# Kernel optimization log

Hardware: AMD Instinct MI355X
Metric: run time of the kernel (lower is better)

The kernel has to match this reference:

```python
import jax, jax.numpy as jnp
import numpy as np

B, D, H, K = 65536, 256, 256, 11
TEMP = 1.0
EPS = 1e-8  # torch cosine_similarity eps


def _gelu(v):
    return jax.nn.gelu(v, approximate=False)  # torch nn.GELU default is exact


def setup_inputs() -> dict:
    key = jax.random.key(0)
    ks = jax.random.split(key, 9)
    s_d = 1.0 / np.sqrt(D)
    s_h = 1.0 / np.sqrt(H)
    return {
        "x": jax.random.normal(ks[0], (B, D), jnp.float32),
        # K transform MLPs, stacked: D->H (gelu) ->D
        "Tw1": jax.random.normal(ks[1], (K, D, H), jnp.float32) * s_d,
        "Tb1": jax.random.normal(ks[2], (K, H), jnp.float32) * 0.01,
        "Tw2": jax.random.normal(ks[3], (K, H, D), jnp.float32) * s_h,
        "Tb2": jax.random.normal(ks[4], (K, D), jnp.float32) * 0.01,
        # encoder MLP: D->H (gelu) ->H
        "Ew1": jax.random.normal(ks[5], (D, H), jnp.float32) * s_d,
        "Eb1": jax.random.normal(ks[6], (H,), jnp.float32) * 0.01,
        "Ew2": jax.random.normal(ks[7], (H, H), jnp.float32) * s_h,
        "Eb2": jax.random.normal(ks[8], (H,), jnp.float32) * 0.01,
    }


def reference(x, Tw1, Tb1, Tw2, Tb2, Ew1, Eb1, Ew2, Eb2):
    def enc(h):  # [..., D] -> [..., H]; dropout is identity at inference
        return _gelu(h @ Ew1 + Eb1) @ Ew2 + Eb2

    # batched transforms: [K, B, D]
    tx = _gelu(jnp.einsum('bd,kdh->kbh', x, Tw1) + Tb1[:, None, :])
    tx = jnp.einsum('kbh,khd->kbd', tx, Tw2) + Tb2[:, None, :]

    z = enc(x)        # [B, H]
    zt = enc(tx)      # [K, B, H]

    nz = jnp.linalg.norm(z, axis=-1)    # [B]
    nzt = jnp.linalg.norm(zt, axis=-1)  # [K, B]

    # exp(cos(z, z_k) / T)  -> [K, B]
    sim_z = jnp.exp(jnp.einsum('bh,kbh->kb', z, zt)
                    / jnp.maximum(nz[None, :] * nzt, EPS) / TEMP)
    # exp(cos(z_l, z_k) / T) -> [K, K, B]
    S = jnp.exp(jnp.einsum('lbh,kbh->lkb', zt, zt)
                / jnp.maximum(nzt[:, None, :] * nzt[None, :, :], EPS) / TEMP)
    diag = jnp.diagonal(S, axis1=0, axis2=1).T  # [K, B]
    neg = S.sum(axis=0) - diag                  # sum over l != k

    scores = jnp.log(sim_z / (sim_z + neg))     # [K, B]
    return -scores.sum(axis=0)                  # [B]
```

## Files before the change

### kernel.cpp

```cpp
#include <hip/hip_runtime.h>
#include <hip/hip_bf16.h>
#include <stdint.h>

#define BTOT  65536
#define KTR   11
#define NSLOT 12

typedef __attribute__((ext_vector_type(8))) short bf16x8_t;
typedef __attribute__((ext_vector_type(4))) float f32x4_t;

__device__ __forceinline__ int act_addr(int m, int n) {
    return m * 256 + ((((n >> 3) + m) & 31) << 3) + (n & 7);
}

__device__ __forceinline__ float gelu_fast(float x) {
    float x2 = x * x;
    float t2 = 2.3022083f * x * fmaf(0.044715f, x2, 1.0f);
    float e  = exp2f(fminf(t2, 44.f));
    return x * e * __builtin_amdgcn_rcpf(1.0f + e);
}

__global__ void cast_x_kernel(const float* __restrict__ x, __hip_bfloat16* __restrict__ xb) {
    int i = (blockIdx.x * 256 + threadIdx.x) * 4;
    float4 v = *(const float4*)(x + i);
    union { __hip_bfloat16 h[4]; uint64_t u; } o;
    o.h[0] = __float2bfloat16(v.x);
    o.h[1] = __float2bfloat16(v.y);
    o.h[2] = __float2bfloat16(v.z);
    o.h[3] = __float2bfloat16(v.w);
    *(uint64_t*)(xb + i) = o.u;
}

__global__ void transpose_cast_kernel(const float* __restrict__ in,
                                      __hip_bfloat16* __restrict__ out,
                                      int R, int C) {
    __shared__ float tile[32][33];
    int tpc = C >> 5;
    int tr = (blockIdx.x / tpc) << 5;
    int tc = (blockIdx.x % tpc) << 5;
    const float* bi = in + (size_t)blockIdx.y * R * C;
    __hip_bfloat16* bo = out + (size_t)blockIdx.y * R * C;
    int lx = threadIdx.x & 31, ly = threadIdx.x >> 5;
    #pragma unroll
    for (int r = 0; r < 32; r += 8)
        tile[ly + r][lx] = bi[(size_t)(tr + ly + r) * C + tc + lx];
    __syncthreads();
    #pragma unroll
    for (int r = 0; r < 32; r += 8)
        bo[(size_t)(tc + ly + r) * R + tr + lx] = __float2bfloat16(tile[lx][ly + r]);
}

__global__ void fuse_w_kernel(const __hip_bfloat16* __restrict__ Ew1t,
                              const __hip_bfloat16* __restrict__ Tw2b,
                              __hip_bfloat16* __restrict__ Wft)
{
    __shared__ __align__(16) __hip_bfloat16 bt[64 * 256];
    const int tid  = threadIdx.x;
    const int wave = tid >> 6, lane = tid & 63;
    const int lr = lane & 15, q = lane >> 4;
    const int k  = blockIdx.y;
    const int h0 = blockIdx.x << 6;
    const __hip_bfloat16* src = Tw2b + (size_t)k * 65536;

    #pragma unroll
    for (int i = 0; i < 8; ++i) {
        int lin = i * 256 + tid;
        int r = lin >> 5, g = lin & 31;
        bf16x8_t v = *(const bf16x8_t*)(src + (size_t)(h0 + r) * 256 + g * 8);
        *(bf16x8_t*)(bt + act_addr(r, g * 8)) = v;
    }
    __syncthreads();

    const int wc = wave << 6;
    f32x4_t acc[4][4];
    #pragma unroll
    for (int mt = 0; mt < 4; ++mt)
        #pragma unroll
        for (int nt = 0; nt < 4; ++nt)
            acc[mt][nt] = (f32x4_t){0.f, 0.f, 0.f, 0.f};

    #pragma unroll 1
    for (int kc = 0; kc < 8; ++kc) {
        const int kof = (kc << 5) + (q << 3);
        bf16x8_t a[4], b[4];
        #pragma unroll
        for (int mt = 0; mt < 4; ++mt)
            a[mt] = *(const bf16x8_t*)(Ew1t + (size_t)(wc + (mt << 4) + lr) * 256 + kof);
        #pragma unroll
        for (int nt = 0; nt < 4; ++nt)
            b[nt] = *(const bf16x8_t*)(bt + act_addr((nt << 4) + lr, kof));
        #pragma unroll
        for (int mt = 0; mt < 4; ++mt)
            #pragma unroll
            for (int nt = 0; nt < 4; ++nt)
                acc[mt][nt] = __builtin_amdgcn_mfma_f32_16x16x32_bf16(a[mt], b[nt], acc[mt][nt], 0, 0, 0);
    }

    __hip_bfloat16* dst = Wft + (size_t)k * 65536;
    #pragma unroll
    for (int mt = 0; mt < 4; ++mt)
        #pragma unroll
        for (int nt = 0; nt < 4; ++nt) {
            const int h = h0 + (nt << 4) + lr;
            #pragma unroll
            for (int r = 0; r < 4; ++r) {
                const int j = wc + (mt << 4) + (q << 2) + r;
                dst[(size_t)j * 256 + h] = __float2bfloat16(acc[mt][nt][r]);
            }
        }
}

__global__ void fuse_b_kernel(const float* __restrict__ Tb2,
                              const float* __restrict__ Ew1,
                              const float* __restrict__ Eb1,
                              float* __restrict__ bf)
{
    const int k = blockIdx.x, j = threadIdx.x;
    float s = Eb1[j];
    #pragma unroll 4
    for (int d = 0; d < 256; ++d)
        s = fmaf(Tb2[k * 256 + d], Ew1[d * 256 + j], s);
    bf[k * 256 + j] = s;
}

template<bool DO_GELU>
__device__ void run_stage(__hip_bfloat16* act,
                          const __hip_bfloat16* __restrict__ Wt,
                          const float* __restrict__ bias,
                          int wave, int lane)
{
    const int lr = lane & 15;
    const int q  = lane >> 4;
    const int wc = wave << 6;

    f32x4_t acc[4][4];
    #pragma unroll
    for (int mt = 0; mt < 4; ++mt) {
        const float4 bv = *(const float4*)(bias + wc + (mt << 4) + (q << 2));
        #pragma unroll
        for (int nt = 0; nt < 4; ++nt)
            acc[mt][nt] = (f32x4_t){bv.x, bv.y, bv.z, bv.w};
    }

    bf16x8_t a[4];
    #pragma unroll
    for (int mt = 0; mt < 4; ++mt)
        a[mt] = *(const bf16x8_t*)(Wt + (size_t)(wc + (mt << 4) + lr) * 256 + (q << 3));

    #pragma unroll 1
    for (int kc = 0; kc < 8; ++kc) {
        const int kof = (kc << 5) + (q << 3);
        bf16x8_t an[4];
        if (kc < 7) {
            #pragma unroll
            for (int mt = 0; mt < 4; ++mt)
                an[mt] = *(const bf16x8_t*)(Wt + (size_t)(wc + (mt << 4) + lr) * 256 + kof + 32);
        }
        bf16x8_t b[4];
        #pragma unroll
        for (int nt = 0; nt < 4; ++nt)
            b[nt] = *(const bf16x8_t*)(act + act_addr((nt << 4) + lr, kof));
        #pragma unroll
        for (int mt = 0; mt < 4; ++mt)
            #pragma unroll
            for (int nt = 0; nt < 4; ++nt)
                acc[mt][nt] = __builtin_amdgcn_mfma_f32_16x16x32_bf16(a[mt], b[nt], acc[mt][nt], 0, 0, 0);
        if (kc < 7) {
            #pragma unroll
            for (int mt = 0; mt < 4; ++mt) a[mt] = an[mt];
        }
    }

    __syncthreads();
    #pragma unroll
    for (int mt = 0; mt < 4; ++mt) {
        const int nbase = wc + (mt << 4) + (q << 2);
        #pragma unroll
        for (int nt = 0; nt < 4; ++nt) {
            const int row = (nt << 4) + lr;
            union { __hip_bfloat16 h[4]; uint64_t u; } o;
            #pragma unroll
            for (int r = 0; r < 4; ++r) {
                float v = acc[mt][nt][r];
                if (DO_GELU) v = gelu_fast(v);
                o.h[r] = __float2bfloat16(v);
            }
            *(uint64_t*)(act + act_addr(row, nbase)) = o.u;
        }
    }
    __syncthreads();
}

__launch_bounds__(256, 3)
__global__ void chain_kernel(const __hip_bfloat16* __restrict__ xb,
                             const __hip_bfloat16* __restrict__ Tw1t,
                             const float* __restrict__ Tb1,
                             const __hip_bfloat16* __restrict__ Wft,
                             const float* __restrict__ bfb,
                             const __hip_bfloat16* __restrict__ Ew1t,
                             const float* __restrict__ Eb1,
                             const __hip_bfloat16* __restrict__ Ew2t,
                             const float* __restrict__ Eb2,
                             __hip_bfloat16* __restrict__ zbuf,
                             int b0)
{
    __shared__ __align__(16) __hip_bfloat16 act[64 * 256];
    const int tid  = threadIdx.x;
    const int wave = tid >> 6, lane = tid & 63;
    const int slot = blockIdx.y;
    const int tile = blockIdx.x;

    #pragma unroll
    for (int i = 0; i < 8; ++i) {
        int lin = i * 256 + tid;
        int r = lin >> 5, g = lin & 31;
        bf16x8_t v = *(const bf16x8_t*)(xb + (size_t)(b0 + tile * 64 + r) * 256 + g * 8);
        *(bf16x8_t*)(act + act_addr(r, g * 8)) = v;
    }
    __syncthreads();

    if (slot < KTR) {
        run_stage<true>(act, Tw1t + (size_t)slot * 65536, Tb1 + slot * 256, wave, lane);
        run_stage<true>(act, Wft  + (size_t)slot * 65536, bfb + slot * 256, wave, lane);
    } else {
        run_stage<true>(act, Ew1t, Eb1, wave, lane);
    }
    run_stage<false>(act, Ew2t, Eb2, wave, lane);

    __hip_bfloat16* dst = zbuf + (size_t)(tile * NSLOT + slot) * (64 * 256);
    #pragma unroll
    for (int i = 0; i < 8; ++i) {
        int lin = i * 256 + tid;
        int r = lin >> 5, g = lin & 31;
        bf16x8_t v = *(const bf16x8_t*)(act + act_addr(r, g * 8));
        __builtin_nontemporal_store(v, (bf16x8_t*)(dst + lin * 8));
    }
}

#define ROW_BODY(V, I)                                                        \
    {                                                                         \
        f32x4_t acc = (f32x4_t){0.f, 0.f, 0.f, 0.f};                          \
        _Pragma("unroll")                                                     \
        for (int kc = 0; kc < 8; ++kc)                                        \
            acc = __builtin_amdgcn_mfma_f32_16x16x32_bf16(V[kc], V[kc], acc, 0, 0, 0); \
        _Pragma("unroll")                                                     \
        for (int rr = 0; rr < 4; ++rr)                                        \
            Gw[wave][(q << 2) + rr][lr] = acc[rr];                            \
        float term = 0.f;                                                     \
        if (lane < 11) {                                                      \
            const int k = lane;                                               \
            float nr[NSLOT];                                                  \
            _Pragma("unroll")                                                 \
            for (int l = 0; l < NSLOT; ++l)                                   \
                nr[l] = __builtin_amdgcn_rcpf(fmaxf(sqrtf(Gw[wave][l][l]), 1e-4f)); \
            const float nrk = nr[k];                                          \
            float neg = 0.f;                                                  \
            _Pragma("unroll")                                                 \
            for (int l = 0; l < KTR; ++l)                                     \
                if (l != k)                                                   \
                    neg += __expf(Gw[wave][l][k] * nr[l] * nrk);              \
            float cz = Gw[wave][KTR][k] * nr[KTR] * nrk;                      \
            term = __logf(__expf(cz) + neg) - cz;                             \
        }                                                                     \
        term += __shfl_xor(term, 1);                                          \
        term += __shfl_xor(term, 2);                                          \
        term += __shfl_xor(term, 4);                                          \
        term += __shfl_xor(term, 8);                                          \
        if (lane == 0) out[b0 + r0 + (I)] = term;                             \
    }

__launch_bounds__(256, 4)
__global__ void reduce_kernel(const __hip_bfloat16* __restrict__ zbuf,
                              float* __restrict__ out, int b0)
{
    __shared__ float Gw[4][16][17];
    const int tid  = threadIdx.x;
    const int wave = tid >> 6, lane = tid & 63;
    const int lr = lane & 15, q = lane >> 4;
    const int slot = lr < NSLOT ? lr : NSLOT - 1;

    const int r0   = (blockIdx.x * 4 + wave) * 8;
    const int tile = r0 >> 6, rloc = r0 & 63;
    const __hip_bfloat16* zr = zbuf + (size_t)tile * (NSLOT * 64 * 256)
                             + (size_t)slot * (64 * 256) + rloc * 256 + (q << 3);

    bf16x8_t va[8], vb[8];
    #pragma unroll
    for (int kc = 0; kc < 8; ++kc)
        va[kc] = __builtin_nontemporal_load((const bf16x8_t*)(zr + kc * 32));

    #pragma unroll 1
    for (int i2 = 0; i2 < 4; ++i2) {
        const int ie = i2 * 2;
        {
            const __hip_bfloat16* zn = zr + (ie + 1) * 256;
            #pragma unroll
            for (int kc = 0; kc < 8; ++kc)
                vb[kc] = __builtin_nontemporal_load((const bf16x8_t*)(zn + kc * 32));
            ROW_BODY(va, ie)
        }
        {
            if (ie + 2 < 8) {
                const __hip_bfloat16* zn = zr + (ie + 2) * 256;
                #pragma unroll
                for (int kc = 0; kc < 8; ++kc)
                    va[kc] = __builtin_nontemporal_load((const bf16x8_t*)(zn + kc * 32));
            }
            ROW_BODY(vb, ie + 1)
        }
    }
}

extern "C" void kernel_launch(void* const* d_in, const int* in_sizes, int n_in,
                              void* d_out, int out_size, void* d_ws, size_t ws_size,
                              hipStream_t stream)
{
    const float* x   = (const float*)d_in[0];
    const float* Tw1 = (const float*)d_in[1];
    const float* Tb1 = (const float*)d_in[2];
    const float* Tw2 = (const float*)d_in[3];
    const float* Tb2 = (const float*)d_in[4];
    const float* Ew1 = (const float*)d_in[5];
    const float* Eb1 = (const float*)d_in[6];
    const float* Ew2 = (const float*)d_in[7];
    const float* Eb2 = (const float*)d_in[8];
    float* out = (float*)d_out;

    char* ws = (char*)d_ws;
    const size_t off_xb   = 0;
    const size_t off_tw1  = off_xb   + (size_t)BTOT * 256 * 2;
    const size_t off_wf   = off_tw1  + (size_t)KTR * 65536 * 2;
    const size_t off_ew1  = off_wf   + (size_t)KTR * 65536 * 2;
    const size_t off_ew2  = off_ew1  + (size_t)65536 * 2;
    const size_t off_tw2b = off_ew2  + (size_t)65536 * 2;
    const size_t off_bf   = off_tw2b + (size_t)KTR * 65536 * 2;
    const size_t off_z    = off_bf   + (size_t)KTR * 256 * 4;

    __hip_bfloat16* xb   = (__hip_bfloat16*)(ws + off_xb);
    __hip_bfloat16* Tw1t = (__hip_bfloat16*)(ws + off_tw1);
    __hip_bfloat16* Wft  = (__hip_bfloat16*)(ws + off_wf);
    __hip_bfloat16* Ew1t = (__hip_bfloat16*)(ws + off_ew1);
    __hip_bfloat16* Ew2t = (__hip_bfloat16*)(ws + off_ew2);
    __hip_bfloat16* Tw2b = (__hip_bfloat16*)(ws + off_tw2b);
    float*          bfb  = (float*)(ws + off_bf);
    __hip_bfloat16* zbuf = (__hip_bfloat16*)(ws + off_z);

    long long zbytes = (long long)ws_size - (long long)off_z;
    long long rows_cap = zbytes > 0 ? zbytes / ((long long)NSLOT * 256 * 2) : 0;
    int chunk = (int)((rows_cap / 128) * 128);
    if (chunk > BTOT / 4) chunk = BTOT / 4;
    if (chunk < 128) chunk = 128;

    cast_x_kernel<<<dim3(BTOT * 256 / 1024), 256, 0, stream>>>(x, xb);
    cast_x_kernel<<<dim3(KTR * 65536 / 1024), 256, 0, stream>>>(Tw2, Tw2b);
    transpose_cast_kernel<<<dim3(64, KTR), 256, 0, stream>>>(Tw1, Tw1t, 256, 256);
    transpose_cast_kernel<<<dim3(64, 1),   256, 0, stream>>>(Ew1, Ew1t, 256, 256);
    transpose_cast_kernel<<<dim3(64, 1),   256, 0, stream>>>(Ew2, Ew2t, 256, 256);
    fuse_b_kernel<<<dim3(KTR), 256, 0, stream>>>(Tb2, Ew1, Eb1, bfb);
    fuse_w_kernel<<<dim3(4, KTR), 256, 0, stream>>>(Ew1t, Tw2b, Wft);

    for (int b0 = 0; b0 < BTOT; b0 += chunk) {
        int rows = (BTOT - b0 < chunk) ? (BTOT - b0) : chunk;
        chain_kernel<<<dim3(rows / 64, NSLOT), 256, 0, stream>>>(
            xb, Tw1t, Tb1, Wft, bfb, Ew1t, Eb1, Ew2t, Eb2, zbuf, b0);
        reduce_kernel<<<dim3(rows / 32), 256, 0, stream>>>(zbuf, out, b0);
    }
}
```

Before: 867.8 us.

## Simplify GELU, split stage into mfma/epilogue parts, raise occupancy and chunk size

Rewrites the tanh-approximation GELU as x*sigmoid form with one fewer multiply and no clamp. Splits run_stage into inlined mfma and epilogue helpers that share one accumulator array declared in the kernel. Raises launch_bounds min blocks per CU from 3 to 4, and doubles the maximum batch chunk so fewer chain/reduce launch pairs are issued. The higher occupancy target may force register spilling given the 64-float accumulator plus prefetch registers, and the unclamped exp2 relies on rcp of infinity giving zero.

```diff
diff --git a/kernel.cpp b/kernel.cpp
--- a/kernel.cpp
+++ b/kernel.cpp
@@ -15,9 +15,9 @@
 
 __device__ __forceinline__ float gelu_fast(float x) {
     float x2 = x * x;
-    float t2 = 2.3022083f * x * fmaf(0.044715f, x2, 1.0f);
-    float e  = exp2f(fminf(t2, 44.f));
-    return x * e * __builtin_amdgcn_rcpf(1.0f + e);
+    float t2 = x * fmaf(0.10294324f, x2, 2.3022083f);
+    float e  = exp2f(-t2);
+    return x * __builtin_amdgcn_rcpf(1.0f + e);
 }
 
 __global__ void cast_x_kernel(const float* __restrict__ x, __hip_bfloat16* __restrict__ xb) {
@@ -123,17 +123,11 @@
     bf[k * 256 + j] = s;
 }
 
-template<bool DO_GELU>
-__device__ void run_stage(__hip_bfloat16* act,
-                          const __hip_bfloat16* __restrict__ Wt,
-                          const float* __restrict__ bias,
-                          int wave, int lane)
-{
-    const int lr = lane & 15;
-    const int q  = lane >> 4;
-    const int wc = wave << 6;
-
-    f32x4_t acc[4][4];
+__device__ __forceinline__ void mfma_part(const __hip_bfloat16* act,
+                                          const __hip_bfloat16* __restrict__ Wt,
+                                          const float* __restrict__ bias,
+                                          f32x4_t acc[4][4], int lr, int q, int wc)
+{
     #pragma unroll
     for (int mt = 0; mt < 4; ++mt) {
         const float4 bv = *(const float4*)(bias + wc + (mt << 4) + (q << 2));
@@ -170,8 +164,12 @@
             for (int mt = 0; mt < 4; ++mt) a[mt] = an[mt];
         }
     }
-
-    __syncthreads();
+}
+
+template<bool DO_GELU>
+__device__ __forceinline__ void ep_part(__hip_bfloat16* act, f32x4_t acc[4][4],
+                                        int lr, int q, int wc)
+{
     #pragma unroll
     for (int mt = 0; mt < 4; ++mt) {
         const int nbase = wc + (mt << 4) + (q << 2);
@@ -188,10 +186,9 @@
             *(uint64_t*)(act + act_addr(row, nbase)) = o.u;
         }
     }
-    __syncthreads();
-}
-
-__launch_bounds__(256, 3)
+}
+
+__launch_bounds__(256, 4)
 __global__ void chain_kernel(const __hip_bfloat16* __restrict__ xb,
                              const __hip_bfloat16* __restrict__ Tw1t,
                              const float* __restrict__ Tb1,
@@ -207,6 +204,7 @@
     __shared__ __align__(16) __hip_bfloat16 act[64 * 256];
     const int tid  = threadIdx.x;
     const int wave = tid >> 6, lane = tid & 63;
+    const int lr = lane & 15, q = lane >> 4, wc = wave << 6;
     const int slot = blockIdx.y;
     const int tile = blockIdx.x;
 
@@ -219,13 +217,26 @@
     }
     __syncthreads();
 
+    f32x4_t acc[4][4];
     if (slot < KTR) {
-        run_stage<true>(act, Tw1t + (size_t)slot * 65536, Tb1 + slot * 256, wave, lane);
-        run_stage<true>(act, Wft  + (size_t)slot * 65536, bfb + slot * 256, wave, lane);
+        mfma_part(act, Tw1t + (size_t)slot * 65536, Tb1 + slot * 256, acc, lr, q, wc);
+        __syncthreads();
+        ep_part<true>(act, acc, lr, q, wc);
+        __syncthreads();
+        mfma_part(act, Wft + (size_t)slot * 65536, bfb + slot * 256, acc, lr, q, wc);
+        __syncthreads();
+        ep_part<true>(act, acc, lr, q, wc);
+        __syncthreads();
     } else {
-        run_stage<true>(act, Ew1t, Eb1, wave, lane);
-    }
-    run_stage<false>(act, Ew2t, Eb2, wave, lane);
+        mfma_part(act, Ew1t, Eb1, acc, lr, q, wc);
+        __syncthreads();
+        ep_part<true>(act, acc, lr, q, wc);
+        __syncthreads();
+    }
+    mfma_part(act, Ew2t, Eb2, acc, lr, q, wc);
+    __syncthreads();
+    ep_part<false>(act, acc, lr, q, wc);
+    __syncthreads();
 
     __hip_bfloat16* dst = zbuf + (size_t)(tile * NSLOT + slot) * (64 * 256);
     #pragma unroll
@@ -348,7 +359,7 @@
     long long zbytes = (long long)ws_size - (long long)off_z;
     long long rows_cap = zbytes > 0 ? zbytes / ((long long)NSLOT * 256 * 2) : 0;
     int chunk = (int)((rows_cap / 128) * 128);
-    if (chunk > BTOT / 4) chunk = BTOT / 4;
+    if (chunk > BTOT / 2) chunk = BTOT / 2;
     if (chunk < 128) chunk = 128;
 
     cast_x_kernel<<<dim3(BTOT * 256 / 1024), 256, 0, stream>>>(x, xb);
```

Measured after the change: 915.9 us. +5.5%, slower.
